# Performance work log

Hardware: AMD Instinct MI355X
Metric: run time of the kernel (lower is better)

Reference implementation:

```python
import jax, jax.numpy as jnp
import numpy as np

PATCH = 14
NPS = 26  # num_patches_per_side = 364 // 14


def setup_inputs() -> dict:
    key = jax.random.key(0)
    k0, k1, k2 = jax.random.split(key, 3)
    B, C, H, W, D = 32, 3, 364, 364, 1152
    pixel_values = jax.random.normal(k0, (B, C, H, W), dtype=jnp.float32)
    # variable-resolution rectangle masks (top-left aligned, NaViT style)
    rng = np.random.default_rng(0)
    nbh = rng.integers(NPS // 2, NPS + 1, size=B)
    nbw = rng.integers(NPS // 2, NPS + 1, size=B)
    mask = np.zeros((B, NPS, NPS), dtype=bool)
    for i in range(B):  # setup-time only, not part of reference compute
        mask[i, : nbh[i], : nbw[i]] = True
    patch_attention_mask = jnp.asarray(mask)
    conv_w = jax.random.normal(k1, (D, C, PATCH, PATCH), dtype=jnp.float32) * 0.02
    conv_b = jnp.zeros((D,), dtype=jnp.float32)
    pos_emb = jax.random.normal(k2, (NPS * NPS, D), dtype=jnp.float32) * 0.02
    return {
        "pixel_values": pixel_values,
        "patch_attention_mask": patch_attention_mask,
        "conv_w": conv_w,
        "conv_b": conv_b,
        "pos_emb": pos_emb,
    }


def _position_ids(mask):
    # mask: [B, Hp, Wp] bool, True on a top-left rectangle per sample
    B, Hp, Wp = mask.shape
    boundaries = jnp.arange(1, NPS, dtype=jnp.float32) / NPS  # NPS-1 edges
    nb_h = mask[:, :, 0].sum(axis=1)  # [B]
    nb_w = mask[:, 0, :].sum(axis=1)  # [B]
    eps = 1.0 - 1e-6
    frac_h = jnp.arange(Hp, dtype=jnp.float32)[None, :] / nb_h[:, None].astype(jnp.float32) * eps
    frac_w = jnp.arange(Wp, dtype=jnp.float32)[None, :] / nb_w[:, None].astype(jnp.float32) * eps
    # torch.bucketize(right=True) == searchsorted side='right'
    bh = jnp.searchsorted(boundaries, frac_h, side="right")  # [B, Hp]
    bw = jnp.searchsorted(boundaries, frac_w, side="right")  # [B, Wp]
    pos = bh[:, :, None] * NPS + bw[:, None, :]  # [B, Hp, Wp]
    pos = pos.reshape(B, Hp * Wp)
    return jnp.where(mask.reshape(B, -1), pos, 0)


def reference(pixel_values, patch_attention_mask, conv_w, conv_b, pos_emb):
    # patch embedding: conv2d stride=patch, padding VALID
    patch_embeds = jax.lax.conv_general_dilated(
        pixel_values, conv_w,
        window_strides=(PATCH, PATCH), padding="VALID",
        dimension_numbers=("NCHW", "OIHW", "NCHW"),
    ) + conv_b[None, :, None, None]  # [B, D, Hp, Wp]
    B, D, Hp, Wp = patch_embeds.shape
    embeddings = patch_embeds.reshape(B, D, Hp * Wp).transpose(0, 2, 1)  # [B, P, D]
    position_ids = _position_ids(patch_attention_mask)  # [B, P]
    return embeddings + pos_emb[position_ids]
```

## Files before the change

kernel.cpp:

```cpp
#include <hip/hip_runtime.h>
#include <stdint.h>

typedef __attribute__((ext_vector_type(8))) short short8;
typedef __attribute__((ext_vector_type(4))) float f32x4;

#define B_      32
#define C_      3
#define HW_     364
#define D_      1152
#define NPS_    26
#define P_      676
#define K_      588
#define KP_     608
#define KC_     19
#define MT_     32
#define NT_     384
#define AS_     616
#define NP_     21632
#define GRID_   676
#define NT16_   72

static __device__ __forceinline__ unsigned short f2bf(float x) {
  unsigned u = __float_as_uint(x);
  u += 0x7fffu + ((u >> 16) & 1u);
  return (unsigned short)(u >> 16);
}

__global__ void prep_weights(const float* __restrict__ w,
                             unsigned short* __restrict__ whi) {
  int idx = blockIdx.x * 256 + threadIdx.x;
  if (idx >= NT16_ * KC_ * 64 * 8) return;
  int e    = idx & 7;
  int lane = (idx >> 3) & 63;
  int t    = idx >> 9;
  int kc   = t % KC_;
  int nt   = t / KC_;
  int n = nt * 16 + (lane & 15);
  int k = kc * 32 + (lane >> 4) * 8 + e;
  float x = (k < K_) ? w[n * K_ + k] : 0.0f;
  whi[idx] = f2bf(x);
}

__global__ void prep_pos(const void* __restrict__ maskp, int* __restrict__ pos_ids) {
  const int word0 = ((const int*)maskp)[0];
  int mode;
  if (word0 == 1) mode = 0;
  else if (word0 == 0x3F800000) mode = 2;
  else mode = 1;

  int idx = blockIdx.x * 256 + threadIdx.x;
  if (idx >= NP_) return;
  const int b = idx / P_;
  const int p = idx - b * P_;
  const int base = b * P_;

  auto get = [&](int i) -> int {
    if (mode == 0) return ((const int*)maskp)[base + i];
    if (mode == 1) return (int)((const unsigned char*)maskp)[base + i];
    return ((const float*)maskp)[base + i] != 0.0f ? 1 : 0;
  };

  int outp = 0;
  if (get(p)) {
    int nbh = 0, nbw = 0;
    #pragma unroll
    for (int r = 0; r < NPS_; ++r) nbh += get(r * NPS_);
    #pragma unroll
    for (int c = 0; c < NPS_; ++c) nbw += get(c);
    const int pr = p / NPS_;
    const int pc = p - pr * NPS_;
    const float eps = 1.0f - 1e-6f;
    const float fh = (float)((double)pr / (double)nbh) * eps;
    const float fw = (float)((double)pc / (double)nbw) * eps;
    int bh = 0, bw = 0;
    #pragma unroll
    for (int k = 1; k < NPS_; ++k) {
      const float bnd = (float)((double)k / (double)NPS_);
      bh += (bnd <= fh) ? 1 : 0;
      bw += (bnd <= fw) ? 1 : 0;
    }
    outp = bh * NPS_ + bw;
  }
  pos_ids[idx] = outp;
}

__global__ __launch_bounds__(512, 8)
void fused_embed(const float* __restrict__ pix,
                 const unsigned short* __restrict__ whi,
                 const float* __restrict__ bias,
                 const float* __restrict__ pos_emb,
                 const int* __restrict__ pos_ids,
                 float* __restrict__ out) {
  __shared__ __align__(16) unsigned short Ahi[MT_ * AS_];

  const int mb  = blockIdx.x;
  const int P0  = mb * MT_;
  const int tid = threadIdx.x;

  for (int task = tid; task < 42 * MT_; task += 512) {
    const int s  = task >> 5;
    const int p  = task & 31;
    const int c  = s / 14;
    const int rr = s - c * 14;
    const int patch = P0 + p;
    const int b  = patch / P_;
    const int pp = patch - b * P_;
    const int pr = pp / NPS_;
    const int pc = pp - pr * NPS_;
    const float* sr = pix + ((size_t)(b * C_ + c) * HW_ + pr * 14 + rr) * HW_ + pc * 14;
    unsigned* dh = (unsigned*)&Ahi[p * AS_ + c * 196 + rr * 14];
    #pragma unroll
    for (int j = 0; j < 7; ++j)
      dh[j] = (unsigned)f2bf(sr[2 * j]) | ((unsigned)f2bf(sr[2 * j + 1]) << 16);
  }
  for (int i = tid; i < MT_ * 14; i += 512) {
    const int p = i / 14;
    const int k = K_ + (i - p * 14) * 2;
    *(unsigned*)(&Ahi[p * AS_ + k]) = 0u;
  }
  __syncthreads();

  const int lane = tid & 63;
  const int wid  = tid >> 6;
  const int l15  = lane & 15;
  const int lk8  = (lane >> 4) << 3;
  const int r4   = (lane >> 4) * 4;

  #pragma unroll 1
  for (int nb = 0; nb < 3; ++nb) {
    const int ntbase = nb * 24 + wid * 3;

    f32x4 acc[2][3];
    #pragma unroll
    for (int mi = 0; mi < 2; ++mi)
      #pragma unroll
      for (int ni = 0; ni < 3; ++ni)
        acc[mi][ni] = (f32x4)0.0f;

    #pragma unroll 1
    for (int kc = 0; kc < KC_; ++kc) {
      const int ko = kc * 32 + lk8;
      short8 ah0 = *(const short8*)&Ahi[l15 * AS_ + ko];
      short8 ah1 = *(const short8*)&Ahi[(16 + l15) * AS_ + ko];
      short8 bh0 = *(const short8*)(whi + (((ntbase + 0) * KC_ + kc) * 64 + lane) * 8);
      short8 bh1 = *(const short8*)(whi + (((ntbase + 1) * KC_ + kc) * 64 + lane) * 8);
      short8 bh2 = *(const short8*)(whi + (((ntbase + 2) * KC_ + kc) * 64 + lane) * 8);
      acc[0][0] = __builtin_amdgcn_mfma_f32_16x16x32_bf16(ah0, bh0, acc[0][0], 0, 0, 0);
      acc[0][1] = __builtin_amdgcn_mfma_f32_16x16x32_bf16(ah0, bh1, acc[0][1], 0, 0, 0);
      acc[0][2] = __builtin_amdgcn_mfma_f32_16x16x32_bf16(ah0, bh2, acc[0][2], 0, 0, 0);
      acc[1][0] = __builtin_amdgcn_mfma_f32_16x16x32_bf16(ah1, bh0, acc[1][0], 0, 0, 0);
      acc[1][1] = __builtin_amdgcn_mfma_f32_16x16x32_bf16(ah1, bh1, acc[1][1], 0, 0, 0);
      acc[1][2] = __builtin_amdgcn_mfma_f32_16x16x32_bf16(ah1, bh2, acc[1][2], 0, 0, 0);
    }

    const int colb = nb * NT_ + wid * 48;
    float cb0 = bias[colb + l15];
    float cb1 = bias[colb + 16 + l15];
    float cb2 = bias[colb + 32 + l15];
    #pragma unroll
    for (int mi = 0; mi < 2; ++mi) {
      #pragma unroll
      for (int r = 0; r < 4; ++r) {
        const int patch = P0 + mi * 16 + r4 + r;
        const int pid = pos_ids[patch];
        const float* pe = pos_emb + (size_t)pid * D_;
        float* po = out + (size_t)patch * D_;
        po[colb + l15]      = acc[mi][0][r] + cb0 + pe[colb + l15];
        po[colb + 16 + l15] = acc[mi][1][r] + cb1 + pe[colb + 16 + l15];
        po[colb + 32 + l15] = acc[mi][2][r] + cb2 + pe[colb + 32 + l15];
      }
    }
  }
}

extern "C" void kernel_launch(void* const* d_in, const int* in_sizes, int n_in,
                              void* d_out, int out_size, void* d_ws, size_t ws_size,
                              hipStream_t stream) {
  const float* pix            = (const float*)d_in[0];
  const void* mask            = (const void*)d_in[1];
  const float* conv_w         = (const float*)d_in[2];
  const float* conv_b         = (const float*)d_in[3];
  const float* pos_emb        = (const float*)d_in[4];
  float* out                  = (float*)d_out;

  char* ws = (char*)d_ws;
  unsigned short* whi = (unsigned short*)ws;
  int* pos_ids        = (int*)(ws + 1400832);

  prep_weights<<<(NT16_ * KC_ * 64 * 8 + 255) / 256, 256, 0, stream>>>(conv_w, whi);
  prep_pos<<<(NP_ + 255) / 256, 256, 0, stream>>>(mask, pos_ids);
  fused_embed<<<GRID_, 512, 0, stream>>>(pix, whi, conv_b, pos_emb, pos_ids, out);
}
```

Baseline: 214.9 us.

## Split N dimension across blocks, swizzle block order, double-buffer fragment loads

Each block now handles one of three column slices for its 32 patches, so the grid grows from 676 to 2028 work items, remapped with a swizzle that spreads consecutive items across XCDs. The K loop is double-buffered: the next chunk's LDS and global weight fragments load while the current chunk's MFMAs run, and the first weight fragment is prefetched before the pixel staging. The cost is that the pixel tile is converted and staged three times, once per column-slice block, and the occupancy hint is lowered to 6.

```diff
diff --git a/kernel.cpp b/kernel.cpp
--- a/kernel.cpp
+++ b/kernel.cpp
@@ -17,7 +17,11 @@
 #define NT_     384
 #define AS_     616
 #define NP_     21632
-#define GRID_   676
+#define MBLK_   676
+#define NBLK_   3
+#define NWORK_  2028
+#define CHUNK_  254
+#define GRID_   2032
 #define NT16_   72
 
 static __device__ __forceinline__ unsigned short f2bf(float x) {
@@ -84,7 +88,41 @@
   pos_ids[idx] = outp;
 }
 
-__global__ __launch_bounds__(512, 8)
+struct Frags { short8 ah[2]; short8 bh[3]; };
+
+__device__ __forceinline__ void load_b(Frags& f, int kc, int ntbase, int lane,
+                                       const unsigned short* __restrict__ whi) {
+  #pragma unroll
+  for (int ni = 0; ni < 3; ++ni) {
+    const int off = (((ntbase + ni) * KC_ + kc) * 64 + lane) * 8;
+    f.bh[ni] = *(const short8*)(whi + off);
+  }
+}
+
+__device__ __forceinline__ void load_a(Frags& f, int kc, int l15, int lk8,
+                                       const unsigned short* Ahi_) {
+  const int ko = kc * 32 + lk8;
+  f.ah[0] = *(const short8*)&Ahi_[l15 * AS_ + ko];
+  f.ah[1] = *(const short8*)&Ahi_[(16 + l15) * AS_ + ko];
+}
+
+__device__ __forceinline__ void load_frags(Frags& f, int kc, int l15, int lk8,
+                                           int ntbase, int lane,
+                                           const unsigned short* Ahi_,
+                                           const unsigned short* __restrict__ whi) {
+  load_a(f, kc, l15, lk8, Ahi_);
+  load_b(f, kc, ntbase, lane, whi);
+}
+
+__device__ __forceinline__ void mfma_frags(f32x4 acc[2][3], const Frags& f) {
+  #pragma unroll
+  for (int mi = 0; mi < 2; ++mi)
+    #pragma unroll
+    for (int ni = 0; ni < 3; ++ni)
+      acc[mi][ni] = __builtin_amdgcn_mfma_f32_16x16x32_bf16(f.ah[mi], f.bh[ni], acc[mi][ni], 0, 0, 0);
+}
+
+__global__ __launch_bounds__(512, 6)
 void fused_embed(const float* __restrict__ pix,
                  const unsigned short* __restrict__ whi,
                  const float* __restrict__ bias,
@@ -93,9 +131,21 @@
                  float* __restrict__ out) {
   __shared__ __align__(16) unsigned short Ahi[MT_ * AS_];
 
-  const int mb  = blockIdx.x;
+  const int bid0 = blockIdx.x;
+  const int w = (bid0 & 7) * CHUNK_ + (bid0 >> 3);
+  if (w >= NWORK_) return;
+  const int mb  = w / NBLK_;
+  const int nb  = w - mb * NBLK_;
   const int P0  = mb * MT_;
   const int tid = threadIdx.x;
+  const int lane = tid & 63;
+  const int wid  = tid >> 6;
+  const int l15  = lane & 15;
+  const int lk8  = (lane >> 4) << 3;
+  const int ntbase = nb * 24 + wid * 3;
+
+  Frags f0, f1;
+  load_b(f0, 0, ntbase, lane, whi);
 
   for (int task = tid; task < 42 * MT_; task += 512) {
     const int s  = task >> 5;
@@ -120,55 +170,39 @@
   }
   __syncthreads();
 
-  const int lane = tid & 63;
-  const int wid  = tid >> 6;
-  const int l15  = lane & 15;
-  const int lk8  = (lane >> 4) << 3;
-  const int r4   = (lane >> 4) * 4;
-
+  f32x4 acc[2][3];
+  #pragma unroll
+  for (int mi = 0; mi < 2; ++mi)
+    #pragma unroll
+    for (int ni = 0; ni < 3; ++ni)
+      acc[mi][ni] = (f32x4)0.0f;
+
+  load_a(f0, 0, l15, lk8, Ahi);
   #pragma unroll 1
-  for (int nb = 0; nb < 3; ++nb) {
-    const int ntbase = nb * 24 + wid * 3;
-
-    f32x4 acc[2][3];
-    #pragma unroll
-    for (int mi = 0; mi < 2; ++mi)
-      #pragma unroll
-      for (int ni = 0; ni < 3; ++ni)
-        acc[mi][ni] = (f32x4)0.0f;
-
-    #pragma unroll 1
-    for (int kc = 0; kc < KC_; ++kc) {
-      const int ko = kc * 32 + lk8;
-      short8 ah0 = *(const short8*)&Ahi[l15 * AS_ + ko];
-      short8 ah1 = *(const short8*)&Ahi[(16 + l15) * AS_ + ko];
-      short8 bh0 = *(const short8*)(whi + (((ntbase + 0) * KC_ + kc) * 64 + lane) * 8);
-      short8 bh1 = *(const short8*)(whi + (((ntbase + 1) * KC_ + kc) * 64 + lane) * 8);
-      short8 bh2 = *(const short8*)(whi + (((ntbase + 2) * KC_ + kc) * 64 + lane) * 8);
-      acc[0][0] = __builtin_amdgcn_mfma_f32_16x16x32_bf16(ah0, bh0, acc[0][0], 0, 0, 0);
-      acc[0][1] = __builtin_amdgcn_mfma_f32_16x16x32_bf16(ah0, bh1, acc[0][1], 0, 0, 0);
-      acc[0][2] = __builtin_amdgcn_mfma_f32_16x16x32_bf16(ah0, bh2, acc[0][2], 0, 0, 0);
-      acc[1][0] = __builtin_amdgcn_mfma_f32_16x16x32_bf16(ah1, bh0, acc[1][0], 0, 0, 0);
-      acc[1][1] = __builtin_amdgcn_mfma_f32_16x16x32_bf16(ah1, bh1, acc[1][1], 0, 0, 0);
-      acc[1][2] = __builtin_amdgcn_mfma_f32_16x16x32_bf16(ah1, bh2, acc[1][2], 0, 0, 0);
-    }
-
-    const int colb = nb * NT_ + wid * 48;
-    float cb0 = bias[colb + l15];
-    float cb1 = bias[colb + 16 + l15];
-    float cb2 = bias[colb + 32 + l15];
-    #pragma unroll
-    for (int mi = 0; mi < 2; ++mi) {
-      #pragma unroll
-      for (int r = 0; r < 4; ++r) {
-        const int patch = P0 + mi * 16 + r4 + r;
-        const int pid = pos_ids[patch];
-        const float* pe = pos_emb + (size_t)pid * D_;
-        float* po = out + (size_t)patch * D_;
-        po[colb + l15]      = acc[mi][0][r] + cb0 + pe[colb + l15];
-        po[colb + 16 + l15] = acc[mi][1][r] + cb1 + pe[colb + 16 + l15];
-        po[colb + 32 + l15] = acc[mi][2][r] + cb2 + pe[colb + 32 + l15];
-      }
+  for (int kc = 0; kc + 2 < KC_; kc += 2) {
+    load_frags(f1, kc + 1, l15, lk8, ntbase, lane, Ahi, whi);
+    mfma_frags(acc, f0);
+    load_frags(f0, kc + 2, l15, lk8, ntbase, lane, Ahi, whi);
+    mfma_frags(acc, f1);
+  }
+  mfma_frags(acc, f0);
+
+  const int colb = nb * NT_ + wid * 48;
+  float cb0 = bias[colb + l15];
+  float cb1 = bias[colb + 16 + l15];
+  float cb2 = bias[colb + 32 + l15];
+  const int r4 = (lane >> 4) * 4;
+  #pragma unroll
+  for (int mi = 0; mi < 2; ++mi) {
+    #pragma unroll
+    for (int r = 0; r < 4; ++r) {
+      const int patch = P0 + mi * 16 + r4 + r;
+      const int pid = pos_ids[patch];
+      const float* pe = pos_emb + (size_t)pid * D_;
+      float* po = out + (size_t)patch * D_;
+      po[colb + l15]      = acc[mi][0][r] + cb0 + pe[colb + l15];
+      po[colb + 16 + l15] = acc[mi][1][r] + cb1 + pe[colb + 16 + l15];
+      po[colb + 32 + l15] = acc[mi][2][r] + cb2 + pe[colb + 32 + l15];
     }
   }
 }
```

Measured after the change: 202.9 us. -5.6%, faster.
